# Optimization experiments

Hardware: AMD Instinct MI355X
Metric: run time of the kernel (lower is better)

The kernel has to match this reference:

```python
import jax, jax.numpy as jnp
import numpy as np

TOP_K = 16  # init kwarg top_k


def setup_inputs() -> dict:
    key = jax.random.key(0)
    ks = jax.random.split(key, 10)
    B, N = 4, 4096
    p = lambda k, shape: jax.random.normal(k, shape, jnp.float32) * 0.05
    return {
        "s": jax.random.normal(ks[0], (B, N, 4), jnp.float32),
        "g": jax.random.normal(ks[1], (B, N, 2), jnp.float32),
        # edge MLP (1x1 convs): 5 -> 64 -> 128  (5 = 4 rel-state + eye flag)
        "w1": p(ks[2], (64, 5)),   "b1": jnp.zeros((64,), jnp.float32),
        "w2": p(ks[3], (128, 64)), "b2": jnp.zeros((128,), jnp.float32),
        # node MLP: 132 -> 64 -> 128 -> 64 -> 4  (132 = 128 pooled + 2 pos-goal + 2 vel)
        "fw1": p(ks[4], (64, 132)), "fb1": jnp.zeros((64,), jnp.float32),
        "fw2": p(ks[5], (128, 64)), "fb2": jnp.zeros((128,), jnp.float32),
        "fw3": p(ks[6], (64, 128)), "fb3": jnp.zeros((64,), jnp.float32),
        "fw4": p(ks[7], (4, 64)),   "fb4": jnp.zeros((4,), jnp.float32),
    }


def reference(s, g, w1, b1, w2, b2, fw1, fb1, fw2, fb2, fw3, fb3, fw4, fb4):
    B, N, D = s.shape
    pos = s[..., :2]                                   # [B,N,2]
    # squared pairwise distances without materializing [B,N,N,2]
    sq = jnp.sum(pos * pos, axis=-1)                   # [B,N]
    d2 = sq[:, :, None] + sq[:, None, :] - 2.0 * jnp.einsum('bnd,bmd->bnm', pos, pos)
    # top_k NEAREST neighbors (includes self, dist 0)
    _, idx = jax.lax.top_k(-d2, TOP_K)                 # idx: [B,N,K]
    # gather neighbor states per batch (avoids [B,N,N,D] blowup)
    nbr = jax.vmap(lambda sb, ib: sb[ib])(s, idx)      # [B,N,K,D]
    rel = s[:, :, None, :] - nbr                       # relative state
    eye = (idx == jnp.arange(N)[None, :, None]).astype(s.dtype)[..., None]
    e = jnp.concatenate([rel, eye], axis=-1)           # [B,N,K,5]
    # shared edge MLP (conv1x1 equivalents)
    h = jax.nn.relu(jnp.einsum('bnkc,oc->bnko', e, w1) + b1)
    h = jax.nn.relu(jnp.einsum('bnkc,oc->bnko', h, w2) + b2)
    feat = jnp.max(h, axis=2)                          # max-pool over neighbors -> [B,N,128]
    node = jnp.concatenate([feat, pos - g, s[..., 2:]], axis=-1)  # [B,N,132]
    h = jax.nn.relu(node @ fw1.T + fb1)
    h = jax.nn.relu(h @ fw2.T + fb2)
    h = jax.nn.relu(h @ fw3.T + fb3)
    out = h @ fw4.T + fb4
    return 2.0 * jax.nn.sigmoid(out) - 1.0             # [B,N,4]
```

## Files before the change

kernel.cpp:

```cpp
#include <hip/hip_runtime.h>
#include <math.h>

#define NPT 4096
#define NTOT 16384

__global__ __launch_bounds__(256) void k0_u(const float* __restrict__ s,
                                            const float* __restrict__ w1,
                                            float* __restrict__ u,
                                            float* __restrict__ w14) {
  int gid = blockIdx.x * 256 + threadIdx.x;
  int n = gid >> 4;
  int c0 = (gid & 15) << 2;
  float4 sv = *(const float4*)(s + (size_t)n * 4);
  float uv[4];
#pragma unroll
  for (int i = 0; i < 4; ++i) {
    const float* wr = w1 + (size_t)(c0 + i) * 5;
    uv[i] = wr[0] * sv.x + wr[1] * sv.y + wr[2] * sv.z + wr[3] * sv.w;
  }
  float4 o; o.x = uv[0]; o.y = uv[1]; o.z = uv[2]; o.w = uv[3];
  *(float4*)(u + (size_t)n * 64 + c0) = o;
  if (blockIdx.x == 0 && threadIdx.x < 64)
    w14[threadIdx.x] = w1[threadIdx.x * 5 + 4];
}

__device__ __forceinline__ unsigned int fkey(float f) {
  unsigned int u = __float_as_uint(f);
  return u ^ ((unsigned int)((int)u >> 31) | 0x80000000u);
}

__global__ __launch_bounds__(256) void k1_knn(const float* __restrict__ s,
                                              unsigned short* __restrict__ knn) {
  __shared__ float2 xy[NPT];
  const int tid = threadIdx.x;
  const int lane = tid & 63;
  const int row = blockIdx.x * 4 + (tid >> 6);
  const int b = row >> 12, n = row & 4095;
  const float* sb = s + (size_t)b * NPT * 4;
  const float INF = __builtin_inff();

#pragma unroll
  for (int j = 0; j < 16; ++j) {
    int idx = tid + j * 256;
    xy[idx] = *(const float2*)(sb + (size_t)idx * 4);
  }
  __syncthreads();

  const float2 pn = xy[n];
  const float sqn = pn.x * pn.x + pn.y * pn.y;

  float m1v = INF, m2v = INF;
  int m1s = 0, m2s = 0;
#pragma unroll 8
  for (int i = 0; i < 64; ++i) {
    float2 pm = xy[i * 64 + lane];
    float sqm = pm.x * pm.x + pm.y * pm.y;
    float dot = pn.x * pm.x + pn.y * pm.y;
    float d2 = (sqn + sqm) - 2.f * dot;
    bool c1 = d2 < m1v;
    bool c2 = d2 < m2v;
    m2v = c1 ? m1v : (c2 ? d2 : m2v);
    m2s = c1 ? m1s : (c2 ? i : m2s);
    m1v = c1 ? d2 : m1v;
    m1s = c1 ? i : m1s;
  }

  unsigned long long lkey =
      ((unsigned long long)fkey(m1v) << 32) | (unsigned)(m1s * 64 + lane);
  unsigned long long k2b =
      ((unsigned long long)fkey(m2v) << 32) | (unsigned)(m2s * 64 + lane);
  bool have2 = true;
  unsigned long long emask = 0;

  for (int r = 0; r < 16; ++r) {
    unsigned long long wk = lkey;
#pragma unroll
    for (int off = 32; off >= 1; off >>= 1) {
      unsigned long long ok =
          (unsigned long long)__shfl_xor((long long)wk, off, 64);
      wk = (ok < wk) ? ok : wk;
    }
    unsigned int m = (unsigned int)wk & 4095u;
    if (lane == r) knn[(size_t)row * 16 + r] = (unsigned short)m;
    if ((int)((unsigned int)wk & 63u) == lane) {
      emask |= 1ull << (m >> 6);
      if (have2) {
        lkey = k2b; have2 = false;
      } else {
        float bv = INF; int bs = 0;
        for (int i = 0; i < 64; ++i) {
          if ((emask >> i) & 1ull) continue;
          float2 pm = xy[i * 64 + lane];
          float sqm = pm.x * pm.x + pm.y * pm.y;
          float dot = pn.x * pm.x + pn.y * pm.y;
          float d2 = (sqn + sqm) - 2.f * dot;
          bool bet = d2 < bv;
          bv = bet ? d2 : bv;
          bs = bet ? i : bs;
        }
        lkey = ((unsigned long long)fkey(bv) << 32) | (unsigned)(bs * 64 + lane);
      }
    }
  }
}

#define DOT4ACC(acc, hv, wv) \
  acc = fmaf((hv).x, (wv).x, fmaf((hv).y, (wv).y, fmaf((hv).z, (wv).z, fmaf((hv).w, (wv).w, acc))))

__global__ __launch_bounds__(256) void k2_edge(
    const float* __restrict__ s, const float* __restrict__ g,
    const float* __restrict__ b1, const float* __restrict__ w2g,
    const float* __restrict__ b2, const float* __restrict__ u,
    const float* __restrict__ w14, const unsigned short* __restrict__ knn,
    float* __restrict__ node) {
  __shared__ float h1T[128 * 68];
  __shared__ float w2T[128 * 68];
  const int tid = threadIdx.x;

  for (int gi = tid; gi < 2048; gi += 256) {
    int o = gi >> 4, ct = gi & 15;
    float4 v = *(const float4*)(w2g + (size_t)gi * 4);
    *(float4*)(w2T + o * 68 + ct * 4) = v;
  }

  {
    const int row = tid >> 1, half = tid & 1, c0 = half * 32;
    const int p = row >> 4, k = row & 15;
    const int n_pt = blockIdx.x * 8 + p;
    const int n_in = n_pt & 4095;
    const int base_b = n_pt - n_in;
    int m_in = knn[(size_t)n_pt * 16 + k] & 4095;
    const float eye = (m_in == n_in) ? 1.f : 0.f;
    const float* un = u + (size_t)n_pt * 64 + c0;
    const float* um = u + (size_t)(base_b + m_in) * 64 + c0;
#pragma unroll
    for (int t = 0; t < 8; ++t) {
      float4 a   = *(const float4*)(un + t * 4);
      float4 bb  = *(const float4*)(um + t * 4);
      float4 b1v = *(const float4*)(b1 + c0 + t * 4);
      float4 wv  = *(const float4*)(w14 + c0 + t * 4);
      float4 h;
      h.x = fmaxf(fmaf(eye, wv.x, (a.x + b1v.x) - bb.x), 0.f);
      h.y = fmaxf(fmaf(eye, wv.y, (a.y + b1v.y) - bb.y), 0.f);
      h.z = fmaxf(fmaf(eye, wv.z, (a.z + b1v.z) - bb.z), 0.f);
      h.w = fmaxf(fmaf(eye, wv.w, (a.w + b1v.w) - bb.w), 0.f);
      *(float4*)(h1T + row * 68 + c0 + t * 4) = h;
    }
  }
  __syncthreads();

  {
    const int p = tid >> 5, oh = tid & 31;
    const int n_pt = blockIdx.x * 8 + p;
    float4 acc[16];
    float4 binit;
    binit.x = b2[oh]; binit.y = b2[oh + 32]; binit.z = b2[oh + 64]; binit.w = b2[oh + 96];
#pragma unroll
    for (int kk = 0; kk < 16; ++kk) acc[kk] = binit;

#pragma unroll 4
    for (int ct = 0; ct < 16; ++ct) {
      float4 w0 = *(const float4*)(w2T + (oh      ) * 68 + ct * 4);
      float4 w1v = *(const float4*)(w2T + (oh + 32) * 68 + ct * 4);
      float4 w2v = *(const float4*)(w2T + (oh + 64) * 68 + ct * 4);
      float4 w3v = *(const float4*)(w2T + (oh + 96) * 68 + ct * 4);
#pragma unroll
      for (int kk = 0; kk < 16; ++kk) {
        float4 hv = *(const float4*)(h1T + (p * 16 + kk) * 68 + ct * 4);
        DOT4ACC(acc[kk].x, hv, w0);
        DOT4ACC(acc[kk].y, hv, w1v);
        DOT4ACC(acc[kk].z, hv, w2v);
        DOT4ACC(acc[kk].w, hv, w3v);
      }
    }
    float4 f = acc[0];
#pragma unroll
    for (int kk = 1; kk < 16; ++kk) {
      f.x = fmaxf(f.x, acc[kk].x); f.y = fmaxf(f.y, acc[kk].y);
      f.z = fmaxf(f.z, acc[kk].z); f.w = fmaxf(f.w, acc[kk].w);
    }
    f.x = fmaxf(f.x, 0.f); f.y = fmaxf(f.y, 0.f);
    f.z = fmaxf(f.z, 0.f); f.w = fmaxf(f.w, 0.f);
    float* nrow = node + (size_t)n_pt * 132;
    nrow[oh] = f.x; nrow[oh + 32] = f.y; nrow[oh + 64] = f.z; nrow[oh + 96] = f.w;
    if (oh == 0) {
      float4 sv = *(const float4*)(s + (size_t)n_pt * 4);
      float2 gv = *(const float2*)(g + (size_t)n_pt * 2);
      nrow[128] = sv.x - gv.x; nrow[129] = sv.y - gv.y;
      nrow[130] = sv.z; nrow[131] = sv.w;
    }
  }
}

__global__ __launch_bounds__(256) void k3_node(
    const float* __restrict__ node,
    const float* __restrict__ fw1, const float* __restrict__ fb1,
    const float* __restrict__ fw2, const float* __restrict__ fb2,
    const float* __restrict__ fw3, const float* __restrict__ fb3,
    const float* __restrict__ fw4, const float* __restrict__ fb4,
    float* __restrict__ out) {
  __shared__ float bufA[32 * 136];
  __shared__ float bufB[32 * 136];
  __shared__ float wb[64 * 136];
  const int tid = threadIdx.x;
  const int n0 = blockIdx.x * 32;
  const int p = tid >> 3, og = tid & 7;

  for (int gi = tid; gi < 32 * 33; gi += 256) {
    int r = gi / 33, ct = gi - r * 33;
    *(float4*)(bufA + r * 136 + ct * 4) = *(const float4*)(node + (size_t)(n0 + r) * 132 + ct * 4);
  }
  for (int gi = tid; gi < 64 * 33; gi += 256) {
    int r = gi / 33, ct = gi - r * 33;
    *(float4*)(wb + r * 136 + ct * 4) = *(const float4*)(fw1 + (size_t)r * 132 + ct * 4);
  }
  __syncthreads();

  {
    float acc[8];
#pragma unroll
    for (int j = 0; j < 8; ++j) acc[j] = fb1[og + 8 * j];
    for (int ct = 0; ct < 33; ++ct) {
      float4 in4 = *(const float4*)(bufA + p * 136 + ct * 4);
#pragma unroll
      for (int j = 0; j < 8; ++j) {
        float4 w4 = *(const float4*)(wb + (og + 8 * j) * 136 + ct * 4);
        DOT4ACC(acc[j], in4, w4);
      }
    }
#pragma unroll
    for (int j = 0; j < 8; ++j) bufB[p * 136 + og + 8 * j] = fmaxf(acc[j], 0.f);
  }
  __syncthreads();
  for (int gi = tid; gi < 128 * 16; gi += 256) {
    int r = gi >> 4, ct = gi & 15;
    *(float4*)(wb + r * 68 + ct * 4) = *(const float4*)(fw2 + (size_t)r * 64 + ct * 4);
  }
  __syncthreads();

  {
    float acc[16];
#pragma unroll
    for (int j = 0; j < 16; ++j) acc[j] = fb2[og + 8 * j];
    for (int ct = 0; ct < 16; ++ct) {
      float4 in4 = *(const float4*)(bufB + p * 136 + ct * 4);
#pragma unroll
      for (int j = 0; j < 16; ++j) {
        float4 w4 = *(const float4*)(wb + (og + 8 * j) * 68 + ct * 4);
        DOT4ACC(acc[j], in4, w4);
      }
    }
#pragma unroll
    for (int j = 0; j < 16; ++j) bufA[p * 136 + og + 8 * j] = fmaxf(acc[j], 0.f);
  }
  __syncthreads();
  for (int gi = tid; gi < 64 * 32; gi += 256) {
    int r = gi >> 5, ct = gi & 31;
    *(float4*)(wb + r * 132 + ct * 4) = *(const float4*)(fw3 + (size_t)r * 128 + ct * 4);
  }
  __syncthreads();

  {
    float acc[8];
#pragma unroll
    for (int j = 0; j < 8; ++j) acc[j] = fb3[og + 8 * j];
    for (int ct = 0; ct < 32; ++ct) {
      float4 in4 = *(const float4*)(bufA + p * 136 + ct * 4);
#pragma unroll
      for (int j = 0; j < 8; ++j) {
        float4 w4 = *(const float4*)(wb + (og + 8 * j) * 132 + ct * 4);
        DOT4ACC(acc[j], in4, w4);
      }
    }
#pragma unroll
    for (int j = 0; j < 8; ++j) bufB[p * 136 + og + 8 * j] = fmaxf(acc[j], 0.f);
  }
  __syncthreads();
  for (int gi = tid; gi < 4 * 16; gi += 256) {
    int r = gi >> 4, ct = gi & 15;
    *(float4*)(wb + r * 68 + ct * 4) = *(const float4*)(fw4 + (size_t)r * 64 + ct * 4);
  }
  __syncthreads();

  if (tid < 128) {
    const int pp = tid >> 2, o = tid & 3;
    float acc = fb4[o];
    for (int ct = 0; ct < 16; ++ct) {
      float4 in4 = *(const float4*)(bufB + pp * 136 + ct * 4);
      float4 w4 = *(const float4*)(wb + o * 68 + ct * 4);
      DOT4ACC(acc, in4, w4);
    }
    float sgm = 1.f / (1.f + expf(-acc));
    out[(size_t)(n0 + pp) * 4 + o] = fmaf(2.f, sgm, -1.f);
  }
}

extern "C" void kernel_launch(void* const* d_in, const int* in_sizes, int n_in,
                              void* d_out, int out_size, void* d_ws, size_t ws_size,
                              hipStream_t stream) {
  (void)in_sizes; (void)n_in; (void)out_size; (void)ws_size;
  const float* s   = (const float*)d_in[0];
  const float* g   = (const float*)d_in[1];
  const float* w1  = (const float*)d_in[2];
  const float* b1  = (const float*)d_in[3];
  const float* w2  = (const float*)d_in[4];
  const float* b2  = (const float*)d_in[5];
  const float* fw1 = (const float*)d_in[6];
  const float* fb1 = (const float*)d_in[7];
  const float* fw2 = (const float*)d_in[8];
  const float* fb2 = (const float*)d_in[9];
  const float* fw3 = (const float*)d_in[10];
  const float* fb3 = (const float*)d_in[11];
  const float* fw4 = (const float*)d_in[12];
  const float* fb4 = (const float*)d_in[13];

  float* ws   = (float*)d_ws;
  float* u    = ws;
  float* w14  = ws + 1048576;
  unsigned short* knn16 = (unsigned short*)(ws + 1048576 + 64);
  float* node = ws + 1048576 + 64 + 131072;
  float* out  = (float*)d_out;

  k0_u   <<<1024, 256, 0, stream>>>(s, w1, u, w14);
  k1_knn <<<4096, 256, 0, stream>>>(s, knn16);
  k2_edge<<<2048, 256, 0, stream>>>(s, g, b1, w2, b2, u, w14, knn16, node);
  k3_node<<<512,  256, 0, stream>>>(node, fw1, fb1, fw2, fb2, fw3, fb3, fw4, fb4, out);
}
```

Measured before the change: 290.7 us.

## Use DPP wave-min reductions and keep top-3 per lane in kNN selection

Replaces the 64-bit shuffle-based butterfly min reduction in the kNN selection with two 32-bit DPP-based wave reductions: a float min over distances followed by an unsigned min over indices for tie-breaking. Each lane now keeps its three best candidates instead of two, so the fallback rescan of a lane's 64 points happens less often. The cost is one more compare/select chain in the main scan and an extra reduction per round. DPP row/broadcast controls are hardware-specific and the result must still match the reference ordering for ties.

```diff
diff --git a/kernel.cpp b/kernel.cpp
--- a/kernel.cpp
+++ b/kernel.cpp
@@ -24,9 +24,27 @@
     w14[threadIdx.x] = w1[threadIdx.x * 5 + 4];
 }
 
-__device__ __forceinline__ unsigned int fkey(float f) {
-  unsigned int u = __float_as_uint(f);
-  return u ^ ((unsigned int)((int)u >> 31) | 0x80000000u);
+#define DPP_STEP_F(ctrl)                                                      \
+  {                                                                           \
+    float t_ = __int_as_float(__builtin_amdgcn_update_dpp(                    \
+        __float_as_int(v), __float_as_int(v), ctrl, 0xf, 0xf, false));        \
+    v = fminf(v, t_);                                                         \
+  }
+__device__ __forceinline__ float wave_min_f32(float v) {
+  DPP_STEP_F(0x111) DPP_STEP_F(0x112) DPP_STEP_F(0x114) DPP_STEP_F(0x118)
+  DPP_STEP_F(0x142) DPP_STEP_F(0x143)
+  return __int_as_float(__builtin_amdgcn_readlane(__float_as_int(v), 63));
+}
+#define DPP_STEP_U(ctrl)                                                      \
+  {                                                                           \
+    unsigned t_ = (unsigned)__builtin_amdgcn_update_dpp(                      \
+        (int)v, (int)v, ctrl, 0xf, 0xf, false);                               \
+    v = (t_ < v) ? t_ : v;                                                    \
+  }
+__device__ __forceinline__ unsigned wave_min_u32(unsigned v) {
+  DPP_STEP_U(0x111) DPP_STEP_U(0x112) DPP_STEP_U(0x114) DPP_STEP_U(0x118)
+  DPP_STEP_U(0x142) DPP_STEP_U(0x143)
+  return (unsigned)__builtin_amdgcn_readlane((int)v, 63);
 }
 
 __global__ __launch_bounds__(256) void k1_knn(const float* __restrict__ s,
@@ -49,56 +67,46 @@
   const float2 pn = xy[n];
   const float sqn = pn.x * pn.x + pn.y * pn.y;
 
-  float m1v = INF, m2v = INF;
-  int m1s = 0, m2s = 0;
+  float s1k = INF, s2k = INF, s3k = INF;
+  unsigned s1m = 0, s2m = 0, s3m = 0;
 #pragma unroll 8
   for (int i = 0; i < 64; ++i) {
-    float2 pm = xy[i * 64 + lane];
+    const unsigned m = (unsigned)(i * 64 + lane);
+    float2 pm = xy[m];
     float sqm = pm.x * pm.x + pm.y * pm.y;
     float dot = pn.x * pm.x + pn.y * pm.y;
     float d2 = (sqn + sqm) - 2.f * dot;
-    bool c1 = d2 < m1v;
-    bool c2 = d2 < m2v;
-    m2v = c1 ? m1v : (c2 ? d2 : m2v);
-    m2s = c1 ? m1s : (c2 ? i : m2s);
-    m1v = c1 ? d2 : m1v;
-    m1s = c1 ? i : m1s;
-  }
-
-  unsigned long long lkey =
-      ((unsigned long long)fkey(m1v) << 32) | (unsigned)(m1s * 64 + lane);
-  unsigned long long k2b =
-      ((unsigned long long)fkey(m2v) << 32) | (unsigned)(m2s * 64 + lane);
-  bool have2 = true;
-  unsigned long long emask = 0;
+    bool c1 = d2 < s1k, c2 = d2 < s2k, c3 = d2 < s3k;
+    s3k = c2 ? s2k : (c3 ? d2 : s3k);  s3m = c2 ? s2m : (c3 ? m : s3m);
+    s2k = c1 ? s1k : (c2 ? d2 : s2k);  s2m = c1 ? s1m : (c2 ? m : s2m);
+    s1k = c1 ? d2 : s1k;               s1m = c1 ? m : s1m;
+  }
+
+  unsigned long long imask = 0;
 
   for (int r = 0; r < 16; ++r) {
-    unsigned long long wk = lkey;
-#pragma unroll
-    for (int off = 32; off >= 1; off >>= 1) {
-      unsigned long long ok =
-          (unsigned long long)__shfl_xor((long long)wk, off, 64);
-      wk = (ok < wk) ? ok : wk;
-    }
-    unsigned int m = (unsigned int)wk & 4095u;
-    if (lane == r) knn[(size_t)row * 16 + r] = (unsigned short)m;
-    if ((int)((unsigned int)wk & 63u) == lane) {
-      emask |= 1ull << (m >> 6);
-      if (have2) {
-        lkey = k2b; have2 = false;
-      } else {
-        float bv = INF; int bs = 0;
+    float kmin = wave_min_f32(s1k);
+    bool ismin = (s1k == kmin);
+    unsigned mc = ismin ? s1m : 0xFFFFFFFFu;
+    unsigned mstar = wave_min_u32(mc);
+    if (lane == r) knn[(size_t)row * 16 + r] = (unsigned short)mstar;
+    if (ismin && s1m == mstar) {
+      imask |= 1ull << (s1m >> 6);
+      s1k = s2k; s1m = s2m; s2k = s3k; s2m = s3m; s3k = INF; s3m = 0;
+      if (s1k == INF) {
+        float bk = INF; unsigned bm = 0;
         for (int i = 0; i < 64; ++i) {
-          if ((emask >> i) & 1ull) continue;
-          float2 pm = xy[i * 64 + lane];
+          if ((imask >> i) & 1ull) continue;
+          unsigned m = (unsigned)(i * 64 + lane);
+          float2 pm = xy[m];
           float sqm = pm.x * pm.x + pm.y * pm.y;
           float dot = pn.x * pm.x + pn.y * pm.y;
           float d2 = (sqn + sqm) - 2.f * dot;
-          bool bet = d2 < bv;
-          bv = bet ? d2 : bv;
-          bs = bet ? i : bs;
+          bool bet = d2 < bk;
+          bk = bet ? d2 : bk;
+          bm = bet ? m : bm;
         }
-        lkey = ((unsigned long long)fkey(bv) << 32) | (unsigned)(bs * 64 + lane);
+        s1k = bk; s1m = bm;
       }
     }
   }
```

After: 234.6 us. 19.3% less time.
